# Performance work log

Hardware: AMD Instinct MI355X
Metric: run time of the kernel (lower is better)

## Reference

```python
import jax, jax.numpy as jnp
import numpy as np

V, E, H, NL = 32000, 400, 1152, 3  # vocab, embed, hidden, layers
T, B = 64, 48


def _uniform(key, shape, std):
    return jax.random.uniform(key, shape, jnp.float32, -std, std)


def setup_inputs() -> dict:
    key = jax.random.key(0)
    ks = jax.random.split(key, 18)
    std = 1.0 / np.sqrt(H)
    inp = {
        "x": jax.random.randint(ks[0], (T, B), 0, V),
        "h0": jnp.zeros((NL, B, H), jnp.float32),
        "c0": jnp.zeros((NL, B, H), jnp.float32),
        "emb_W": jax.random.normal(ks[1], (V, E), jnp.float32) * 0.02,
        # layer 0: input E -> 4H ; layers 1,2: H -> 4H
        "W_i0": _uniform(ks[2], (4 * H, E), std), "b_i0": _uniform(ks[3], (4 * H,), std),
        "W_h0": _uniform(ks[4], (4 * H, H), std), "b_h0": _uniform(ks[5], (4 * H,), std),
        "W_i1": _uniform(ks[6], (4 * H, H), std), "b_i1": _uniform(ks[7], (4 * H,), std),
        "W_h1": _uniform(ks[8], (4 * H, H), std), "b_h1": _uniform(ks[9], (4 * H,), std),
        "W_i2": _uniform(ks[10], (4 * H, H), std), "b_i2": _uniform(ks[11], (4 * H,), std),
        "W_h2": _uniform(ks[12], (4 * H, H), std), "b_h2": _uniform(ks[13], (4 * H,), std),
        "W_dec": _uniform(ks[14], (V, H), 1.0 / np.sqrt(H)),
        "b_dec": _uniform(ks[15], (V,), 1.0 / np.sqrt(H)),
    }
    return inp


def _cell(z, h, c, Wi, bi, Wh, bh):
    # preact: [B, 4H]; gate layout per the original: i | f | o | g
    p = z @ Wi.T + bi + h @ Wh.T + bh
    i = jax.nn.sigmoid(p[:, :H])
    f = jax.nn.sigmoid(p[:, H:2 * H])
    o = jax.nn.sigmoid(p[:, 2 * H:3 * H])
    g = jnp.tanh(p[:, 3 * H:])
    c_t = f * c + i * g
    h_t = o * jnp.tanh(c_t)
    return h_t, c_t


def reference(x, h0, c0, emb_W,
              W_i0, b_i0, W_h0, b_h0,
              W_i1, b_i1, W_h1, b_h1,
              W_i2, b_i2, W_h2, b_h2,
              W_dec, b_dec):
    # eval-mode forward: dropout / drop-connect / variational dropout are identity
    emb = emb_W[x]  # [T, B, E]

    def step(carry, xt):
        ha, ca, hb, cb, hc, cc = carry
        ha, ca = _cell(xt, ha, ca, W_i0, b_i0, W_h0, b_h0)
        hb, cb = _cell(ha, hb, cb, W_i1, b_i1, W_h1, b_h1)
        hc, cc = _cell(hb, hc, cc, W_i2, b_i2, W_h2, b_h2)
        return (ha, ca, hb, cb, hc, cc), hc

    carry0 = (h0[0], c0[0], h0[1], c0[1], h0[2], c0[2])
    (ha, ca, hb, cb, hc, cc), out = jax.lax.scan(step, carry0, emb)  # out: [T, B, H]
    decoded = jnp.einsum('tbh,vh->tbv', out, W_dec) + b_dec  # [T, B, V]
    h_fin = jnp.stack([ha, hb, hc])
    c_fin = jnp.stack([ca, cb, cc])
    return decoded, (h_fin, c_fin)
```

## Files before the change

### kernel.cpp

```cpp
#include <hip/hip_runtime.h>

typedef unsigned short u16;
typedef __attribute__((ext_vector_type(8))) short s16x8;
typedef __attribute__((ext_vector_type(4))) float f32x4;

#define T_ 64
#define B_ 48
#define H_ 1152
#define E_ 400
#define EPAD 416
#define V_ 32000
#define FOURH 4608
#define TB_ 3072
#define HB (B_*H_)
#define LSTRIDE (65*HB)
#define RBLK 512

#define OFF_ZPRE0 ((size_t)0)
#define OFF_HHI   ((size_t)56623104)
#define OFF_HLO   ((size_t)78188544)
#define OFF_CST   ((size_t)99753984)
#define OFF_ZH    ((size_t)100417536)
#define OFF_ZL    ((size_t)102973440)
#define OFF_PA    ((size_t)105529344)
#define OFF_PB    ((size_t)108183552)
#define OFF_CTR   ((size_t)110837760)

__device__ __forceinline__ u16 f2bf(float x) {
    unsigned u = __float_as_uint(x);
    u += 0x7fffu + ((u >> 16) & 1u);
    return (u16)(u >> 16);
}
__device__ __forceinline__ float bf2f(u16 h) {
    return __uint_as_float(((unsigned)h) << 16);
}
__device__ __forceinline__ void split8(const float* p, s16x8& hi, s16x8& lo) {
    f32x4 a = *(const f32x4*)(p);
    f32x4 b = *(const f32x4*)(p + 4);
    float v[8];
#pragma unroll
    for (int j = 0; j < 4; ++j) { v[j] = a[j]; v[j + 4] = b[j]; }
#pragma unroll
    for (int j = 0; j < 8; ++j) {
        u16 h = f2bf(v[j]);
        hi[j] = (short)h;
        lo[j] = (short)f2bf(v[j] - bf2f(h));
    }
}
__device__ __forceinline__ f32x4 mfma16(s16x8 a, s16x8 b, f32x4 c) {
    return __builtin_amdgcn_mfma_f32_16x16x32_bf16(a, b, c, 0, 0, 0);
}

__device__ __forceinline__ float ld_sc(const float* p) {
    return __hip_atomic_load(p, __ATOMIC_RELAXED, __HIP_MEMORY_SCOPE_AGENT);
}
__device__ __forceinline__ void st_sc(float* p, float v) {
    __hip_atomic_store(p, v, __ATOMIC_RELAXED, __HIP_MEMORY_SCOPE_AGENT);
}
__device__ __forceinline__ void st_sc16(u16* p, u16 v) {
    __hip_atomic_store(p, v, __ATOMIC_RELAXED, __HIP_MEMORY_SCOPE_AGENT);
}

__device__ __forceinline__ void grid_barrier(int* cnt, int* gen, int nblk) {
    asm volatile("s_waitcnt vmcnt(0)" ::: "memory");
    __syncthreads();
    if (threadIdx.x == 0) {
        int g = __hip_atomic_load(gen, __ATOMIC_RELAXED, __HIP_MEMORY_SCOPE_AGENT);
        int old = __hip_atomic_fetch_add(cnt, 1, __ATOMIC_RELAXED, __HIP_MEMORY_SCOPE_AGENT);
        if (old == nblk - 1) {
            __hip_atomic_store(cnt, 0, __ATOMIC_RELAXED, __HIP_MEMORY_SCOPE_AGENT);
            asm volatile("s_waitcnt vmcnt(0)" ::: "memory");
            __hip_atomic_fetch_add(gen, 1, __ATOMIC_RELAXED, __HIP_MEMORY_SCOPE_AGENT);
        } else {
            while (__hip_atomic_load(gen, __ATOMIC_RELAXED, __HIP_MEMORY_SCOPE_AGENT) == g) {
                __builtin_amdgcn_s_sleep(2);
            }
        }
    }
    __syncthreads();
}

__global__ void gather_split_kernel(const int* __restrict__ x, const float* __restrict__ embW,
                                    u16* __restrict__ Zh, u16* __restrict__ Zl) {
    int i = blockIdx.x * blockDim.x + threadIdx.x;
    const int total = TB_ * EPAD;
    if (i >= total) return;
    int tb = i / EPAD, k = i - tb * EPAD;
    float v = 0.f;
    if (k < E_) v = embW[(size_t)x[tb] * E_ + k];
    u16 h = f2bf(v);
    Zh[i] = h;
    Zl[i] = f2bf(v - bf2f(h));
}

__global__ void init_state_kernel(const float* __restrict__ h0, const float* __restrict__ c0,
                                  u16* __restrict__ Hhi, u16* __restrict__ Hlo,
                                  float* __restrict__ Cst) {
    int i = blockIdx.x * blockDim.x + threadIdx.x;
    if (i >= 3 * HB) return;
    int l = i / HB, r = i - l * HB;
    float h = h0[i];
    u16 hh = f2bf(h);
    size_t idx = (size_t)l * LSTRIDE + r;
    Hhi[idx] = hh;
    Hlo[idx] = f2bf(h - bf2f(hh));
    Cst[i] = c0[i];
}

__global__ __launch_bounds__(256, 2) void gemm_bias_kernel(
    const u16* __restrict__ Ahi, const u16* __restrict__ Alo, int lda,
    const float* __restrict__ W, int ldw, int kvalid, int ksteps,
    const float* __restrict__ bias1, const float* __restrict__ bias2,
    float* __restrict__ C, int ldc) {
    const int lane = threadIdx.x & 63;
    const int wv = threadIdx.x >> 6;
    const int m16 = lane & 15, q = lane >> 4;
    const int mbase = blockIdx.y * 192 + wv * 48;
    const int nbase = blockIdx.x * 128;

    f32x4 acc[8][3];
#pragma unroll
    for (int s8 = 0; s8 < 8; ++s8)
#pragma unroll
        for (int mt = 0; mt < 3; ++mt) acc[s8][mt] = (f32x4){0.f, 0.f, 0.f, 0.f};

    const u16* arow[3];
    const u16* alrow[3];
#pragma unroll
    for (int mt = 0; mt < 3; ++mt) {
        size_t m = (size_t)(mbase + mt * 16 + m16);
        arow[mt] = Ahi + m * lda + q * 8;
        alrow[mt] = Alo + m * lda + q * 8;
    }
    const float* wrow[8];
#pragma unroll
    for (int s8 = 0; s8 < 8; ++s8) {
        size_t n = (size_t)(nbase + s8 * 16 + m16);
        wrow[s8] = W + n * ldw + q * 8;
    }

    for (int ks = 0; ks < ksteps; ++ks) {
        int k = ks * 32;
        s16x8 ah[3], al[3];
#pragma unroll
        for (int mt = 0; mt < 3; ++mt) {
            ah[mt] = *(const s16x8*)(arow[mt] + k);
            al[mt] = *(const s16x8*)(alrow[mt] + k);
        }
        int kk = k + q * 8;
#pragma unroll
        for (int s8 = 0; s8 < 8; ++s8) {
            s16x8 wh, wl;
            if (kk + 8 <= kvalid) {
                split8(wrow[s8] + k, wh, wl);
            } else {
#pragma unroll
                for (int j = 0; j < 8; ++j) { wh[j] = 0; wl[j] = 0; }
            }
#pragma unroll
            for (int mt = 0; mt < 3; ++mt) {
                acc[s8][mt] = mfma16(ah[mt], wh, acc[s8][mt]);
                acc[s8][mt] = mfma16(ah[mt], wl, acc[s8][mt]);
                acc[s8][mt] = mfma16(al[mt], wh, acc[s8][mt]);
            }
        }
    }
#pragma unroll
    for (int s8 = 0; s8 < 8; ++s8) {
        int n = nbase + s8 * 16 + m16;
        float bv = (bias1 ? bias1[n] : 0.f) + (bias2 ? bias2[n] : 0.f);
#pragma unroll
        for (int mt = 0; mt < 3; ++mt)
#pragma unroll
            for (int r = 0; r < 4; ++r) {
                int m = mbase + mt * 16 + q * 4 + r;
                C[(size_t)m * ldc + n] = acc[s8][mt][r] + bv;
            }
    }
}

__global__ __launch_bounds__(256, 2) void recur_kernel(
    const float* __restrict__ Wh0, const float* __restrict__ Wi1, const float* __restrict__ Wh1,
    const float* __restrict__ Wi2, const float* __restrict__ Wh2,
    const float* __restrict__ bi0, const float* __restrict__ bh0,
    const float* __restrict__ bi1, const float* __restrict__ bh1,
    const float* __restrict__ bi2, const float* __restrict__ bh2,
    const float* __restrict__ Zpre0, u16* __restrict__ Hhi, u16* __restrict__ Hlo,
    float* __restrict__ Cst, float* __restrict__ Pa, float* __restrict__ Pb,
    int* __restrict__ ctrs, float* __restrict__ out_h, float* __restrict__ out_c) {
    const int lane = threadIdx.x & 63;
    const int slot = threadIdx.x >> 6;
    const int blk = blockIdx.x;
    const int m16 = lane & 15, q = lane >> 4;
    int* cnt = ctrs + 0;
    int* gen = ctrs + 1;

    for (int s = 0; s < 66; ++s) {
        const int t0 = s, t1 = s - 1, t2 = s - 2;
        int units[5];
        int nu = 0;
        if (t0 >= 0 && t0 < 64) units[nu++] = 0;
        if (t1 >= 0 && t1 < 64) { units[nu++] = 1; units[nu++] = 2; }
        if (t2 >= 0 && t2 < 64) { units[nu++] = 3; units[nu++] = 4; }
        const int ntasks = nu * 288;
        const int jj = (slot - blk) & 3;
        const int task = jj * RBLK + blk;
        if (task < ntasks) {
            const int u = units[task / 288];
            const int strip = task % 288;
            const int n0 = strip * 16;
            int tt;
            size_t aoff;
            const float* W;
            float* Pout;
            bool initZ = false;
            switch (u) {
                case 0: tt = t0; W = Wh0; aoff = (size_t)tt * HB;                 Pout = Pa;                       initZ = true; break;
                case 1: tt = t1; W = Wi1; aoff = (size_t)(tt + 1) * HB;           Pout = Pa + (size_t)B_ * FOURH;  break;
                case 2: tt = t1; W = Wh1; aoff = LSTRIDE + (size_t)tt * HB;       Pout = Pb + (size_t)B_ * FOURH;  break;
                case 3: tt = t2; W = Wi2; aoff = LSTRIDE + (size_t)(tt + 1) * HB; Pout = Pa + 2 * (size_t)B_ * FOURH; break;
                default: tt = t2; W = Wh2; aoff = 2 * (size_t)LSTRIDE + (size_t)tt * HB; Pout = Pb + 2 * (size_t)B_ * FOURH; break;
            }
            f32x4 acc[3];
            if (initZ) {
                const float* zp = Zpre0 + (size_t)(tt * B_) * FOURH + n0 + m16;
#pragma unroll
                for (int mt = 0; mt < 3; ++mt)
#pragma unroll
                    for (int r = 0; r < 4; ++r)
                        acc[mt][r] = zp[(size_t)(mt * 16 + q * 4 + r) * FOURH];
            } else {
#pragma unroll
                for (int mt = 0; mt < 3; ++mt) acc[mt] = (f32x4){0.f, 0.f, 0.f, 0.f};
            }
            const float* wrow = W + (size_t)(n0 + m16) * H_ + q * 8;
            const u16* arow[3];
            const u16* alrow[3];
#pragma unroll
            for (int mt = 0; mt < 3; ++mt) {
                size_t ro = aoff + (size_t)(mt * 16 + m16) * H_ + q * 8;
                arow[mt] = Hhi + ro;
                alrow[mt] = Hlo + ro;
            }
#pragma unroll 2
            for (int ks = 0; ks < 36; ++ks) {
                int k = ks * 32;
                s16x8 wh, wl;
                split8(wrow + k, wh, wl);
#pragma unroll
                for (int mt = 0; mt < 3; ++mt) {
                    s16x8 ah = *(const s16x8*)(arow[mt] + k);
                    s16x8 al = *(const s16x8*)(alrow[mt] + k);
                    acc[mt] = mfma16(ah, wh, acc[mt]);
                    acc[mt] = mfma16(ah, wl, acc[mt]);
                    acc[mt] = mfma16(al, wh, acc[mt]);
                }
            }
            float* pout = Pout + n0 + m16;
#pragma unroll
            for (int mt = 0; mt < 3; ++mt)
#pragma unroll
                for (int r = 0; r < 4; ++r)
                    st_sc(pout + (size_t)(mt * 16 + q * 4 + r) * FOURH, acc[mt][r]);
        }
        grid_barrier(cnt, gen, RBLK);

        int actl[3];
        int nl = 0;
        if (t0 >= 0 && t0 < 64) actl[nl++] = 0;
        if (t1 >= 0 && t1 < 64) actl[nl++] = 1;
        if (t2 >= 0 && t2 < 64) actl[nl++] = 2;
        const int nitems = nl * HB;
        for (int i = blk * 256 + threadIdx.x; i < nitems; i += RBLK * 256) {
            int li = i / HB, r = i - li * HB;
            int l = actl[li];
            int tt = s - l;
            int b = r / H_, j = r - b * H_;
            const float* pa = Pa + (size_t)l * B_ * FOURH + (size_t)b * FOURH;
            float pi = ld_sc(pa + j), pf = ld_sc(pa + H_ + j);
            float po = ld_sc(pa + 2 * H_ + j), pg = ld_sc(pa + 3 * H_ + j);
            if (l > 0) {
                const float* pb = Pb + (size_t)l * B_ * FOURH + (size_t)b * FOURH;
                pi += ld_sc(pb + j); pf += ld_sc(pb + H_ + j);
                po += ld_sc(pb + 2 * H_ + j); pg += ld_sc(pb + 3 * H_ + j);
            }
            const float* bi = (l == 0) ? bi0 : (l == 1) ? bi1 : bi2;
            const float* bh = (l == 0) ? bh0 : (l == 1) ? bh1 : bh2;
            pi += bi[j] + bh[j];
            pf += bi[H_ + j] + bh[H_ + j];
            po += bi[2 * H_ + j] + bh[2 * H_ + j];
            pg += bi[3 * H_ + j] + bh[3 * H_ + j];
            float c = ld_sc(Cst + l * HB + r);
            float ig = 1.f / (1.f + expf(-pi));
            float fg = 1.f / (1.f + expf(-pf));
            float og = 1.f / (1.f + expf(-po));
            float gg = tanhf(pg);
            float cn = fg * c + ig * gg;
            float hn = og * tanhf(cn);
            st_sc(Cst + l * HB + r, cn);
            u16 hh = f2bf(hn);
            size_t hidx = (size_t)l * LSTRIDE + (size_t)(tt + 1) * HB + r;
            st_sc16(Hhi + hidx, hh);
            st_sc16(Hlo + hidx, f2bf(hn - bf2f(hh)));
            if (tt == 63) {
                out_h[l * HB + r] = hn;
                out_c[l * HB + r] = cn;
            }
        }
        grid_barrier(cnt, gen, RBLK);
    }
}

extern "C" void kernel_launch(void* const* d_in, const int* in_sizes, int n_in,
                              void* d_out, int out_size, void* d_ws, size_t ws_size,
                              hipStream_t stream) {
    (void)in_sizes; (void)n_in; (void)out_size; (void)ws_size;
    const int* x = (const int*)d_in[0];
    const float* h0 = (const float*)d_in[1];
    const float* c0 = (const float*)d_in[2];
    const float* embW = (const float*)d_in[3];
    const float* Wi0 = (const float*)d_in[4];
    const float* bi0 = (const float*)d_in[5];
    const float* Wh0 = (const float*)d_in[6];
    const float* bh0 = (const float*)d_in[7];
    const float* Wi1 = (const float*)d_in[8];
    const float* bi1 = (const float*)d_in[9];
    const float* Wh1 = (const float*)d_in[10];
    const float* bh1 = (const float*)d_in[11];
    const float* Wi2 = (const float*)d_in[12];
    const float* bi2 = (const float*)d_in[13];
    const float* Wh2 = (const float*)d_in[14];
    const float* bh2 = (const float*)d_in[15];
    const float* Wdec = (const float*)d_in[16];
    const float* bdec = (const float*)d_in[17];

    char* ws = (char*)d_ws;
    float* Zpre0 = (float*)(ws + OFF_ZPRE0);
    u16* Hhi = (u16*)(ws + OFF_HHI);
    u16* Hlo = (u16*)(ws + OFF_HLO);
    float* Cst = (float*)(ws + OFF_CST);
    u16* Zh = (u16*)(ws + OFF_ZH);
    u16* Zl = (u16*)(ws + OFF_ZL);
    float* Pa = (float*)(ws + OFF_PA);
    float* Pb = (float*)(ws + OFF_PB);
    int* ctrs = (int*)(ws + OFF_CTR);

    float* decoded = (float*)d_out;
    float* out_h = decoded + (size_t)TB_ * V_;
    float* out_c = out_h + 3 * (size_t)HB;

    hipMemsetAsync(ctrs, 0, 256 * sizeof(int), stream);
    gather_split_kernel<<<(TB_ * EPAD + 255) / 256, 256, 0, stream>>>(x, embW, Zh, Zl);
    init_state_kernel<<<(3 * HB + 255) / 256, 256, 0, stream>>>(h0, c0, Hhi, Hlo, Cst);

    dim3 gA(FOURH / 128, TB_ / 192);
    gemm_bias_kernel<<<gA, 256, 0, stream>>>(Zh, Zl, EPAD, Wi0, E_, E_, (E_ + 31) / 32,
                                             nullptr, nullptr, Zpre0, FOURH);

    recur_kernel<<<RBLK, 256, 0, stream>>>(Wh0, Wi1, Wh1, Wi2, Wh2,
                                           bi0, bh0, bi1, bh1, bi2, bh2,
                                           Zpre0, Hhi, Hlo, Cst, Pa, Pb, ctrs, out_h, out_c);

    dim3 gD(V_ / 128, TB_ / 192);
    gemm_bias_kernel<<<gD, 256, 0, stream>>>(Hhi + (size_t)(2 * 65 + 1) * HB,
                                             Hlo + (size_t)(2 * 65 + 1) * HB, H_,
                                             Wdec, H_, H_, H_ / 32,
                                             bdec, nullptr, decoded, V_);
}
```

Baseline: 8.193 ms.

## Split recurrent GEMM along K, double block count, use hierarchical grid barrier

Each recurrent GEMM strip is split into two K halves, which doubles the task count. The persistent grid grows to 1024 blocks at 4 blocks per CU, and the gate-combine step now sums the two partial buffers. The inner K loop software-prefetches weights two steps ahead and activations one step ahead. The grid barrier becomes a two-level tree over 16 group counters so fewer blocks contend on one atomic. The costs are extra partial-sum stores and loads, more register pressure under the tighter launch bound, and the need for 1024 blocks to be co-resident.

Measured after the change: 7.695 ms. -6.1%, faster.

```diff
diff --git a/kernel.cpp b/kernel.cpp
--- a/kernel.cpp
+++ b/kernel.cpp
@@ -14,7 +14,8 @@
 #define TB_ 3072
 #define HB (B_*H_)
 #define LSTRIDE (65*HB)
-#define RBLK 512
+#define RBLK 1024
+#define PSZ ((size_t)(3*B_*FOURH))
 
 #define OFF_ZPRE0 ((size_t)0)
 #define OFF_HHI   ((size_t)56623104)
@@ -22,9 +23,8 @@
 #define OFF_CST   ((size_t)99753984)
 #define OFF_ZH    ((size_t)100417536)
 #define OFF_ZL    ((size_t)102973440)
-#define OFF_PA    ((size_t)105529344)
-#define OFF_PB    ((size_t)108183552)
-#define OFF_CTR   ((size_t)110837760)
+#define OFF_P0    ((size_t)105529344)
+#define OFF_CTR   ((size_t)116146176)
 
 __device__ __forceinline__ u16 f2bf(float x) {
     unsigned u = __float_as_uint(x);
@@ -47,6 +47,17 @@
         lo[j] = (short)f2bf(v[j] - bf2f(h));
     }
 }
+__device__ __forceinline__ void split8r(f32x4 a, f32x4 b, s16x8& hi, s16x8& lo) {
+    float v[8];
+#pragma unroll
+    for (int j = 0; j < 4; ++j) { v[j] = a[j]; v[j + 4] = b[j]; }
+#pragma unroll
+    for (int j = 0; j < 8; ++j) {
+        u16 h = f2bf(v[j]);
+        hi[j] = (short)h;
+        lo[j] = (short)f2bf(v[j] - bf2f(h));
+    }
+}
 __device__ __forceinline__ f32x4 mfma16(s16x8 a, s16x8 b, f32x4 c) {
     return __builtin_amdgcn_mfma_f32_16x16x32_bf16(a, b, c, 0, 0, 0);
 }
@@ -61,20 +72,28 @@
     __hip_atomic_store(p, v, __ATOMIC_RELAXED, __HIP_MEMORY_SCOPE_AGENT);
 }
 
-__device__ __forceinline__ void grid_barrier(int* cnt, int* gen, int nblk) {
+__device__ __forceinline__ void grid_barrier(int* ctrs, int nblk) {
     asm volatile("s_waitcnt vmcnt(0)" ::: "memory");
     __syncthreads();
     if (threadIdx.x == 0) {
+        int* gen = ctrs + 252;
+        int* root = ctrs + 248;
+        int* gcnt = ctrs + ((blockIdx.x & 15) << 4);
+        const int gsz = nblk >> 4;
         int g = __hip_atomic_load(gen, __ATOMIC_RELAXED, __HIP_MEMORY_SCOPE_AGENT);
-        int old = __hip_atomic_fetch_add(cnt, 1, __ATOMIC_RELAXED, __HIP_MEMORY_SCOPE_AGENT);
-        if (old == nblk - 1) {
-            __hip_atomic_store(cnt, 0, __ATOMIC_RELAXED, __HIP_MEMORY_SCOPE_AGENT);
+        int old = __hip_atomic_fetch_add(gcnt, 1, __ATOMIC_RELAXED, __HIP_MEMORY_SCOPE_AGENT);
+        if (old == gsz - 1) {
+            __hip_atomic_store(gcnt, 0, __ATOMIC_RELAXED, __HIP_MEMORY_SCOPE_AGENT);
             asm volatile("s_waitcnt vmcnt(0)" ::: "memory");
-            __hip_atomic_fetch_add(gen, 1, __ATOMIC_RELAXED, __HIP_MEMORY_SCOPE_AGENT);
-        } else {
-            while (__hip_atomic_load(gen, __ATOMIC_RELAXED, __HIP_MEMORY_SCOPE_AGENT) == g) {
-                __builtin_amdgcn_s_sleep(2);
-            }
+            int r = __hip_atomic_fetch_add(root, 1, __ATOMIC_RELAXED, __HIP_MEMORY_SCOPE_AGENT);
+            if (r == 15) {
+                __hip_atomic_store(root, 0, __ATOMIC_RELAXED, __HIP_MEMORY_SCOPE_AGENT);
+                asm volatile("s_waitcnt vmcnt(0)" ::: "memory");
+                __hip_atomic_fetch_add(gen, 1, __ATOMIC_RELAXED, __HIP_MEMORY_SCOPE_AGENT);
+            }
+        }
+        while (__hip_atomic_load(gen, __ATOMIC_RELAXED, __HIP_MEMORY_SCOPE_AGENT) == g) {
+            __builtin_amdgcn_s_sleep(4);
         }
     }
     __syncthreads();
@@ -179,21 +198,19 @@
     }
 }
 
-__global__ __launch_bounds__(256, 2) void recur_kernel(
+__global__ __launch_bounds__(256, 4) void recur_kernel(
     const float* __restrict__ Wh0, const float* __restrict__ Wi1, const float* __restrict__ Wh1,
     const float* __restrict__ Wi2, const float* __restrict__ Wh2,
     const float* __restrict__ bi0, const float* __restrict__ bh0,
     const float* __restrict__ bi1, const float* __restrict__ bh1,
     const float* __restrict__ bi2, const float* __restrict__ bh2,
     const float* __restrict__ Zpre0, u16* __restrict__ Hhi, u16* __restrict__ Hlo,
-    float* __restrict__ Cst, float* __restrict__ Pa, float* __restrict__ Pb,
+    float* __restrict__ Cst, float* __restrict__ P0,
     int* __restrict__ ctrs, float* __restrict__ out_h, float* __restrict__ out_c) {
     const int lane = threadIdx.x & 63;
     const int slot = threadIdx.x >> 6;
     const int blk = blockIdx.x;
     const int m16 = lane & 15, q = lane >> 4;
-    int* cnt = ctrs + 0;
-    int* gen = ctrs + 1;
 
     for (int s = 0; s < 66; ++s) {
         const int t0 = s, t1 = s - 1, t2 = s - 2;
@@ -202,25 +219,34 @@
         if (t0 >= 0 && t0 < 64) units[nu++] = 0;
         if (t1 >= 0 && t1 < 64) { units[nu++] = 1; units[nu++] = 2; }
         if (t2 >= 0 && t2 < 64) { units[nu++] = 3; units[nu++] = 4; }
-        const int ntasks = nu * 288;
+        const int ntasks = nu * 576;
         const int jj = (slot - blk) & 3;
         const int task = jj * RBLK + blk;
         if (task < ntasks) {
-            const int u = units[task / 288];
-            const int strip = task % 288;
+            const int u = units[task / 576];
+            const int rem = task % 576;
+            const int kh = rem & 1;
+            const int strip = rem >> 1;
             const int n0 = strip * 16;
+            const int koff = kh * 576;
             int tt;
             size_t aoff;
             const float* W;
             float* Pout;
             bool initZ = false;
             switch (u) {
-                case 0: tt = t0; W = Wh0; aoff = (size_t)tt * HB;                 Pout = Pa;                       initZ = true; break;
-                case 1: tt = t1; W = Wi1; aoff = (size_t)(tt + 1) * HB;           Pout = Pa + (size_t)B_ * FOURH;  break;
-                case 2: tt = t1; W = Wh1; aoff = LSTRIDE + (size_t)tt * HB;       Pout = Pb + (size_t)B_ * FOURH;  break;
-                case 3: tt = t2; W = Wi2; aoff = LSTRIDE + (size_t)(tt + 1) * HB; Pout = Pa + 2 * (size_t)B_ * FOURH; break;
-                default: tt = t2; W = Wh2; aoff = 2 * (size_t)LSTRIDE + (size_t)tt * HB; Pout = Pb + 2 * (size_t)B_ * FOURH; break;
-            }
+                case 0: tt = t0; W = Wh0; aoff = (size_t)tt * HB;
+                        Pout = P0 + 2 * PSZ;                          initZ = (kh == 0); break;
+                case 1: tt = t1; W = Wi1; aoff = (size_t)(tt + 1) * HB;
+                        Pout = P0 + (size_t)B_ * FOURH;               break;
+                case 2: tt = t1; W = Wh1; aoff = LSTRIDE + (size_t)tt * HB;
+                        Pout = P0 + 2 * PSZ + (size_t)B_ * FOURH;     break;
+                case 3: tt = t2; W = Wi2; aoff = LSTRIDE + (size_t)(tt + 1) * HB;
+                        Pout = P0 + 2 * (size_t)B_ * FOURH;           break;
+                default: tt = t2; W = Wh2; aoff = 2 * (size_t)LSTRIDE + (size_t)tt * HB;
+                        Pout = P0 + 2 * PSZ + 2 * (size_t)B_ * FOURH; break;
+            }
+            if (kh) Pout += PSZ;
             f32x4 acc[3];
             if (initZ) {
                 const float* zp = Zpre0 + (size_t)(tt * B_) * FOURH + n0 + m16;
@@ -233,28 +259,49 @@
 #pragma unroll
                 for (int mt = 0; mt < 3; ++mt) acc[mt] = (f32x4){0.f, 0.f, 0.f, 0.f};
             }
-            const float* wrow = W + (size_t)(n0 + m16) * H_ + q * 8;
+            const float* wrow = W + (size_t)(n0 + m16) * H_ + koff + q * 8;
             const u16* arow[3];
             const u16* alrow[3];
 #pragma unroll
             for (int mt = 0; mt < 3; ++mt) {
-                size_t ro = aoff + (size_t)(mt * 16 + m16) * H_ + q * 8;
+                size_t ro = aoff + (size_t)(mt * 16 + m16) * H_ + koff + q * 8;
                 arow[mt] = Hhi + ro;
                 alrow[mt] = Hlo + ro;
             }
+            f32x4 w0A = *(const f32x4*)(wrow);
+            f32x4 w0B = *(const f32x4*)(wrow + 4);
+            f32x4 w1A = *(const f32x4*)(wrow + 32);
+            f32x4 w1B = *(const f32x4*)(wrow + 36);
+            s16x8 ah[3], al[3];
+#pragma unroll
+            for (int mt = 0; mt < 3; ++mt) {
+                ah[mt] = *(const s16x8*)(arow[mt]);
+                al[mt] = *(const s16x8*)(alrow[mt]);
+            }
 #pragma unroll 2
-            for (int ks = 0; ks < 36; ++ks) {
-                int k = ks * 32;
+            for (int ks = 0; ks < 18; ++ks) {
+                int kp1 = ks + 1; if (kp1 > 17) kp1 = 17;
+                int kp2 = ks + 2; if (kp2 > 17) kp2 = 17;
+                const int kn1 = kp1 * 32, kn2 = kp2 * 32;
+                f32x4 w2A = *(const f32x4*)(wrow + kn2);
+                f32x4 w2B = *(const f32x4*)(wrow + kn2 + 4);
+                s16x8 nah[3], nal[3];
+#pragma unroll
+                for (int mt = 0; mt < 3; ++mt) {
+                    nah[mt] = *(const s16x8*)(arow[mt] + kn1);
+                    nal[mt] = *(const s16x8*)(alrow[mt] + kn1);
+                }
                 s16x8 wh, wl;
-                split8(wrow + k, wh, wl);
+                split8r(w0A, w0B, wh, wl);
 #pragma unroll
                 for (int mt = 0; mt < 3; ++mt) {
-                    s16x8 ah = *(const s16x8*)(arow[mt] + k);
-                    s16x8 al = *(const s16x8*)(alrow[mt] + k);
-                    acc[mt] = mfma16(ah, wh, acc[mt]);
-                    acc[mt] = mfma16(ah, wl, acc[mt]);
-                    acc[mt] = mfma16(al, wh, acc[mt]);
+                    acc[mt] = mfma16(ah[mt], wh, acc[mt]);
+                    acc[mt] = mfma16(ah[mt], wl, acc[mt]);
+                    acc[mt] = mfma16(al[mt], wh, acc[mt]);
                 }
+                w0A = w1A; w0B = w1B; w1A = w2A; w1B = w2B;
+#pragma unroll
+                for (int mt = 0; mt < 3; ++mt) { ah[mt] = nah[mt]; al[mt] = nal[mt]; }
             }
             float* pout = Pout + n0 + m16;
 #pragma unroll
@@ -263,7 +310,7 @@
                 for (int r = 0; r < 4; ++r)
                     st_sc(pout + (size_t)(mt * 16 + q * 4 + r) * FOURH, acc[mt][r]);
         }
-        grid_barrier(cnt, gen, RBLK);
+        grid_barrier(ctrs, RBLK);
 
         int actl[3];
         int nl = 0;
@@ -276,13 +323,19 @@
             int l = actl[li];
             int tt = s - l;
             int b = r / H_, j = r - b * H_;
-            const float* pa = Pa + (size_t)l * B_ * FOURH + (size_t)b * FOURH;
-            float pi = ld_sc(pa + j), pf = ld_sc(pa + H_ + j);
-            float po = ld_sc(pa + 2 * H_ + j), pg = ld_sc(pa + 3 * H_ + j);
+            const float* p2 = P0 + 2 * PSZ + (size_t)l * B_ * FOURH + (size_t)b * FOURH;
+            const float* p3 = p2 + PSZ;
+            float pi = ld_sc(p2 + j) + ld_sc(p3 + j);
+            float pf = ld_sc(p2 + H_ + j) + ld_sc(p3 + H_ + j);
+            float po = ld_sc(p2 + 2 * H_ + j) + ld_sc(p3 + 2 * H_ + j);
+            float pg = ld_sc(p2 + 3 * H_ + j) + ld_sc(p3 + 3 * H_ + j);
             if (l > 0) {
-                const float* pb = Pb + (size_t)l * B_ * FOURH + (size_t)b * FOURH;
-                pi += ld_sc(pb + j); pf += ld_sc(pb + H_ + j);
-                po += ld_sc(pb + 2 * H_ + j); pg += ld_sc(pb + 3 * H_ + j);
+                const float* pz0 = P0 + (size_t)l * B_ * FOURH + (size_t)b * FOURH;
+                const float* pz1 = pz0 + PSZ;
+                pi += ld_sc(pz0 + j) + ld_sc(pz1 + j);
+                pf += ld_sc(pz0 + H_ + j) + ld_sc(pz1 + H_ + j);
+                po += ld_sc(pz0 + 2 * H_ + j) + ld_sc(pz1 + 2 * H_ + j);
+                pg += ld_sc(pz0 + 3 * H_ + j) + ld_sc(pz1 + 3 * H_ + j);
             }
             const float* bi = (l == 0) ? bi0 : (l == 1) ? bi1 : bi2;
             const float* bh = (l == 0) ? bh0 : (l == 1) ? bh1 : bh2;
@@ -307,7 +360,7 @@
                 out_c[l * HB + r] = cn;
             }
         }
-        grid_barrier(cnt, gen, RBLK);
+        grid_barrier(ctrs, RBLK);
     }
 }
 
@@ -341,8 +394,7 @@
     float* Cst = (float*)(ws + OFF_CST);
     u16* Zh = (u16*)(ws + OFF_ZH);
     u16* Zl = (u16*)(ws + OFF_ZL);
-    float* Pa = (float*)(ws + OFF_PA);
-    float* Pb = (float*)(ws + OFF_PB);
+    float* P0 = (float*)(ws + OFF_P0);
     int* ctrs = (int*)(ws + OFF_CTR);
 
     float* decoded = (float*)d_out;
@@ -359,7 +411,7 @@
 
     recur_kernel<<<RBLK, 256, 0, stream>>>(Wh0, Wi1, Wh1, Wi2, Wh2,
                                            bi0, bh0, bi1, bh1, bi2, bh2,
-                                           Zpre0, Hhi, Hlo, Cst, Pa, Pb, ctrs, out_h, out_c);
+                                           Zpre0, Hhi, Hlo, Cst, P0, ctrs, out_h, out_c);
 
     dim3 gD(V_ / 128, TB_ / 192);
     gemm_bias_kernel<<<gD, 256, 0, stream>>>(Hhi + (size_t)(2 * 65 + 1) * HB,
```
